# Kernel tuning notes

Hardware: AMD Instinct MI355X
Metric: run time of the kernel (lower is better)

## Reference

```python
import jax, jax.numpy as jnp
import numpy as np

E = 8          # num_experts
TOP_K = 2      # num_experts_per_tok
H = 1024       # hidden_size
F = 2048       # intermediate_size
B, S = 2, 4096


def setup_inputs() -> dict:
    key = jax.random.key(0)
    ks = jax.random.split(key, 5)
    hidden_states = jax.random.normal(ks[0], (B, S, H), dtype=jnp.float32)
    gate_w = jax.random.normal(ks[1], (E, H), dtype=jnp.float32) * 0.02   # router: logits = x @ gate_w.T
    Wg = jax.random.normal(ks[2], (E, H, F), dtype=jnp.float32) * 0.02    # gate_proj per expert
    Wu = jax.random.normal(ks[3], (E, H, F), dtype=jnp.float32) * 0.02    # up_proj per expert
    Wd = jax.random.normal(ks[4], (E, F, H), dtype=jnp.float32) * 0.02    # down_proj per expert
    return {"hidden_states": hidden_states, "gate_w": gate_w, "Wg": Wg, "Wu": Wu, "Wd": Wd}


def reference(hidden_states, gate_w, Wg, Wu, Wd):
    b, s, h = hidden_states.shape
    x = hidden_states.reshape(-1, h)                       # [T, H]
    T = x.shape[0]

    router_logits = x @ gate_w.T                           # [T, E]
    probs = jax.nn.softmax(router_logits.astype(jnp.float32), axis=-1)
    topk_w, topk_idx = jax.lax.top_k(probs, TOP_K)         # [T, K]
    topk_w = topk_w / jnp.sum(topk_w, axis=-1, keepdims=True)  # norm_topk_prob
    topk_w = topk_w.astype(x.dtype)

    # Dense per-token-per-expert combine weight (0 for unselected experts).
    w_full = jnp.zeros((T, E), dtype=x.dtype)
    w_full = w_full.at[jnp.arange(T)[:, None], topk_idx].add(topk_w)  # [T, E]

    out = jnp.zeros_like(x)
    for e in range(E):  # fixed small loop over experts
        g = jax.nn.silu(x @ Wg[e]) * (x @ Wu[e])           # [T, F]
        out = out + w_full[:, e:e + 1] * (g @ Wd[e])       # [T, H]

    return out.reshape(b, s, h), router_logits
```

## Files before the change

### kernel.cpp

```cpp
#include <hip/hip_runtime.h>
#include <cstdint>

#define NTOK   8192
#define HDIM   1024
#define FDIM   2048
#define NEXP   8
#define RTOT   (2*NTOK)
#define RPAD   128

typedef unsigned short u16;
typedef short   bf16x8 __attribute__((ext_vector_type(8)));
typedef float   f32x4  __attribute__((ext_vector_type(4)));
typedef u16     u16x8  __attribute__((ext_vector_type(8)));

__device__ __forceinline__ u16 f2bf(float v) {
  union { float f; uint32_t u; } a; a.f = v;
  uint32_t r = a.u + 0x7FFFu + ((a.u >> 16) & 1u);
  return (u16)(r >> 16);
}
__device__ __forceinline__ float bf2f(u16 b) {
  union { uint32_t u; float f; } a; a.u = ((uint32_t)b) << 16; return a.f;
}

__global__ void router_kernel(const float* __restrict__ x, const float* __restrict__ gw,
                              float* __restrict__ logits, int* __restrict__ te,
                              float* __restrict__ tw) {
  int gid  = blockIdx.x * blockDim.x + threadIdx.x;
  int t    = gid >> 6;
  int lane = gid & 63;
  const float4* xr = (const float4*)(x + (size_t)t * HDIM);
  float acc[NEXP];
#pragma unroll
  for (int e = 0; e < NEXP; ++e) acc[e] = 0.f;
#pragma unroll
  for (int c = 0; c < 4; ++c) {
    float4 xv = xr[c * 64 + lane];
#pragma unroll
    for (int e = 0; e < NEXP; ++e) {
      float4 wv = ((const float4*)(gw + e * HDIM))[c * 64 + lane];
      acc[e] += xv.x * wv.x + xv.y * wv.y + xv.z * wv.z + xv.w * wv.w;
    }
  }
#pragma unroll
  for (int off = 32; off > 0; off >>= 1)
#pragma unroll
    for (int e = 0; e < NEXP; ++e) acc[e] += __shfl_xor(acc[e], off, 64);

  if (lane == 0) {
#pragma unroll
    for (int e = 0; e < NEXP; ++e) logits[(size_t)t * NEXP + e] = acc[e];
    int e1 = 0;
#pragma unroll
    for (int e = 1; e < NEXP; ++e) if (acc[e] > acc[e1]) e1 = e;
    int e2 = -1;
#pragma unroll
    for (int e = 0; e < NEXP; ++e) {
      if (e == e1) continue;
      if (e2 < 0 || acc[e] > acc[e2]) e2 = e;
    }
    float m  = fmaxf(acc[e1], acc[e2]);
    float p1 = __expf(acc[e1] - m), p2 = __expf(acc[e2] - m);
    float inv = 1.f / (p1 + p2);
    te[t * 2]     = e1;  tw[t * 2]     = p1 * inv;
    te[t * 2 + 1] = e2;  tw[t * 2 + 1] = p2 * inv;
  }
}

__global__ void count_prefix_kernel(const int* __restrict__ te, int* __restrict__ offs,
                                    int* __restrict__ cursors) {
  __shared__ int wsum[16][NEXP];
  int cnt[NEXP];
#pragma unroll
  for (int e = 0; e < NEXP; ++e) cnt[e] = 0;
  for (int i = threadIdx.x; i < 2 * NTOK; i += 1024) {
    int v = te[i];
#pragma unroll
    for (int e = 0; e < NEXP; ++e) cnt[e] += (v == e) ? 1 : 0;
  }
#pragma unroll
  for (int off = 32; off > 0; off >>= 1)
#pragma unroll
    for (int e = 0; e < NEXP; ++e) cnt[e] += __shfl_xor(cnt[e], off, 64);
  int wave = threadIdx.x >> 6, lane = threadIdx.x & 63;
  if (lane == 0)
#pragma unroll
    for (int e = 0; e < NEXP; ++e) wsum[wave][e] = cnt[e];
  __syncthreads();
  if (threadIdx.x == 0) {
    int s = 0;
    for (int e = 0; e < NEXP; ++e) {
      int c = 0;
      for (int w = 0; w < 16; ++w) c += wsum[w][e];
      offs[e] = s; cursors[e * 16] = s; s += c;
    }
    offs[NEXP] = s;
  }
}

__global__ void scatter_kernel(const int* __restrict__ te, const float* __restrict__ tw,
                               int* __restrict__ cursors, int* __restrict__ tok_ids,
                               float* __restrict__ wts, int* __restrict__ slots) {
  int t    = blockIdx.x * blockDim.x + threadIdx.x;
  int lane = threadIdx.x & 63;
#pragma unroll
  for (int s = 0; s < 2; ++s) {
    int   e = te[t * 2 + s];
    float w = tw[t * 2 + s];
    int pos = 0;
#pragma unroll
    for (int e0 = 0; e0 < NEXP; ++e0) {
      unsigned long long m = __ballot(e == e0);
      if (e == e0) {
        int leader = __ffsll((unsigned long long)m) - 1;
        int rank   = __popcll(m & ((1ull << lane) - 1ull));
        int b = 0;
        if (lane == leader) b = atomicAdd(&cursors[e0 * 16], (int)__popcll(m));
        b = __shfl(b, leader, 64);
        pos = b + rank;
      }
    }
    tok_ids[pos] = t;
    wts[pos] = w;
    slots[t * 2 + s] = pos;
  }
}

__global__ void gather_cast_kernel(const float* __restrict__ x, const int* __restrict__ tok_ids,
                                   u16* __restrict__ Xg) {
  int j = blockIdx.x;
  int t = tok_ids[j];
  float4 v = ((const float4*)(x + (size_t)t * HDIM))[threadIdx.x];
  ushort4 o;
  o.x = f2bf(v.x); o.y = f2bf(v.y); o.z = f2bf(v.z); o.w = f2bf(v.w);
  ((ushort4*)(Xg + (size_t)j * HDIM))[threadIdx.x] = o;
}

__global__ __launch_bounds__(256)
void prep_weights_kernel(const float* __restrict__ Wg, const float* __restrict__ Wu,
                         const float* __restrict__ Wd, u16* __restrict__ Wgt,
                         u16* __restrict__ Wut, u16* __restrict__ Wdt) {
  __shared__ float tile[64 * 65];
  const int mat = blockIdx.z >> 3;
  const int e   = blockIdx.z & 7;
  const int K   = (mat < 2) ? HDIM : FDIM;
  const int N   = (mat < 2) ? FDIM : HDIM;
  const float* src = ((mat == 0) ? Wg : (mat == 1) ? Wu : Wd) + (size_t)e * K * N;
  u16*         dst = ((mat == 0) ? Wgt : (mat == 1) ? Wut : Wdt) + (size_t)e * K * N;
  const int tn = (mat < 2) ? blockIdx.x : blockIdx.y;
  const int tk = (mat < 2) ? blockIdx.y : blockIdx.x;
  const int k0 = tk * 64, n0 = tn * 64;

  const int r  = threadIdx.x >> 2;
  const int c4 = threadIdx.x & 3;
#pragma unroll
  for (int i = 0; i < 4; ++i) {
    int c = (c4 + i * 4) * 4;
    float4 v = *(const float4*)(src + (size_t)(k0 + r) * N + n0 + c);
    tile[r * 65 + c]     = v.x;
    tile[r * 65 + c + 1] = v.y;
    tile[r * 65 + c + 2] = v.z;
    tile[r * 65 + c + 3] = v.w;
  }
  __syncthreads();

  const int kq = threadIdx.x & 7;
  const int nr = threadIdx.x >> 3;
#pragma unroll
  for (int p = 0; p < 2; ++p) {
    int n = p * 32 + nr;
    u16x8 pk;
#pragma unroll
    for (int j = 0; j < 8; ++j)
      pk[j] = f2bf(tile[(kq * 8 + j) * 65 + n]);
    *(u16x8*)(dst + (size_t)(n0 + n) * K + k0 + kq * 8) = pk;
  }
}

__device__ __forceinline__ void stage_tile(const u16* __restrict__ src, int ld,
                                           u16* __restrict__ lds, int wave, int lane) {
#pragma unroll
  for (int i = 0; i < 4; ++i) {
    int chunk = ((i << 2) + wave) << 9;
    int flat  = chunk + (lane << 3);
    int row   = flat >> 6;
    int km    = (flat & 63) ^ ((row & 7) << 3);
    __builtin_amdgcn_global_load_lds(
        (const __attribute__((address_space(1))) uint32_t*)(src + (size_t)row * ld + km),
        (__attribute__((address_space(3))) uint32_t*)(lds + chunk),
        16, 0, 0);
  }
}

__global__ __launch_bounds__(256, 2)
void gemm1_kernel(const u16* __restrict__ Xg, const u16* __restrict__ Wgt,
                  const u16* __restrict__ Wut, const int* __restrict__ offs,
                  u16* __restrict__ G) {
  const int e     = blockIdx.z;
  const int rbase = offs[e];
  const int rows  = offs[e + 1] - rbase;
  const int row0  = blockIdx.y * 128;
  if (row0 >= rows) return;
  const int n0    = blockIdx.x * 128;
  const int arow0 = rbase + row0;

  __shared__ __align__(16) u16 As[128 * 64];
  __shared__ __align__(16) u16 Bgs[128 * 64];
  __shared__ __align__(16) u16 Bus[128 * 64];

  const int tid  = threadIdx.x;
  const int wave = tid >> 6;
  const int lane = tid & 63;
  const int wm   = wave >> 1, wn = wave & 1;
  const int l15  = lane & 15, quad = lane >> 4;

  const u16* Ag = Xg  + (size_t)arow0 * HDIM;
  const u16* Bg = Wgt + (size_t)e * FDIM * HDIM + (size_t)n0 * HDIM;
  const u16* Bu = Wut + (size_t)e * FDIM * HDIM + (size_t)n0 * HDIM;

  f32x4 accg[4][4], accu[4][4];
#pragma unroll
  for (int i = 0; i < 4; ++i)
#pragma unroll
    for (int j = 0; j < 4; ++j) { accg[i][j] = (f32x4)0.f; accu[i][j] = (f32x4)0.f; }

  for (int kt = 0; kt < HDIM / 64; ++kt) {
    const int k0 = kt * 64;
    stage_tile(Ag + k0, HDIM, As,  wave, lane);
    stage_tile(Bg + k0, HDIM, Bgs, wave, lane);
    stage_tile(Bu + k0, HDIM, Bus, wave, lane);
    __syncthreads();
#pragma unroll
    for (int kk = 0; kk < 64; kk += 32) {
      bf16x8 af[4];
#pragma unroll
      for (int im = 0; im < 4; ++im) {
        int r  = wm * 64 + im * 16 + l15;
        int kq = (kk + quad * 8) ^ ((r & 7) << 3);
        af[im] = *(const bf16x8*)(As + r * 64 + kq);
      }
#pragma unroll
      for (int in = 0; in < 4; ++in) {
        int r  = wn * 64 + in * 16 + l15;
        int kq = (kk + quad * 8) ^ ((r & 7) << 3);
        bf16x8 bg = *(const bf16x8*)(Bgs + r * 64 + kq);
        bf16x8 bu = *(const bf16x8*)(Bus + r * 64 + kq);
#pragma unroll
        for (int im = 0; im < 4; ++im) {
          accg[im][in] = __builtin_amdgcn_mfma_f32_16x16x32_bf16(af[im], bg, accg[im][in], 0, 0, 0);
          accu[im][in] = __builtin_amdgcn_mfma_f32_16x16x32_bf16(af[im], bu, accu[im][in], 0, 0, 0);
        }
      }
    }
    __syncthreads();
  }

#pragma unroll
  for (int im = 0; im < 4; ++im) {
#pragma unroll
    for (int rr = 0; rr < 4; ++rr) {
      int lrow = row0 + wm * 64 + im * 16 + quad * 4 + rr;
      if (lrow < rows) {
        size_t grow = (size_t)(rbase + lrow);
#pragma unroll
        for (int in = 0; in < 4; ++in) {
          float g = accg[im][in][rr];
          float u = accu[im][in][rr];
          float val = g / (1.f + __expf(-g)) * u;
          int gcol = n0 + wn * 64 + in * 16 + l15;
          G[grow * FDIM + gcol] = f2bf(val);
        }
      }
    }
  }
}

__global__ __launch_bounds__(256, 2)
void gemm2_kernel(const u16* __restrict__ G, const u16* __restrict__ Wdt,
                  const int* __restrict__ offs, const float* __restrict__ wts,
                  u16* __restrict__ Y) {
  const int e     = blockIdx.z;
  const int rbase = offs[e];
  const int rows  = offs[e + 1] - rbase;
  const int row0  = blockIdx.y * 128;
  if (row0 >= rows) return;
  const int n0    = blockIdx.x * 128;
  const int arow0 = rbase + row0;

  __shared__ __align__(16) u16 As[128 * 64];
  __shared__ __align__(16) u16 Bs[128 * 64];

  const int tid  = threadIdx.x;
  const int wave = tid >> 6;
  const int lane = tid & 63;
  const int wm   = wave >> 1, wn = wave & 1;
  const int l15  = lane & 15, quad = lane >> 4;

  const u16* Ag = G   + (size_t)arow0 * FDIM;
  const u16* Bg = Wdt + (size_t)e * HDIM * FDIM + (size_t)n0 * FDIM;

  f32x4 acc[4][4];
#pragma unroll
  for (int i = 0; i < 4; ++i)
#pragma unroll
    for (int j = 0; j < 4; ++j) acc[i][j] = (f32x4)0.f;

  for (int kt = 0; kt < FDIM / 64; ++kt) {
    const int k0 = kt * 64;
    stage_tile(Ag + k0, FDIM, As, wave, lane);
    stage_tile(Bg + k0, FDIM, Bs, wave, lane);
    __syncthreads();
#pragma unroll
    for (int kk = 0; kk < 64; kk += 32) {
      bf16x8 af[4], bf[4];
#pragma unroll
      for (int im = 0; im < 4; ++im) {
        int r  = wm * 64 + im * 16 + l15;
        int kq = (kk + quad * 8) ^ ((r & 7) << 3);
        af[im] = *(const bf16x8*)(As + r * 64 + kq);
      }
#pragma unroll
      for (int in = 0; in < 4; ++in) {
        int r  = wn * 64 + in * 16 + l15;
        int kq = (kk + quad * 8) ^ ((r & 7) << 3);
        bf[in] = *(const bf16x8*)(Bs + r * 64 + kq);
      }
#pragma unroll
      for (int in = 0; in < 4; ++in)
#pragma unroll
        for (int im = 0; im < 4; ++im)
          acc[im][in] = __builtin_amdgcn_mfma_f32_16x16x32_bf16(af[im], bf[in], acc[im][in], 0, 0, 0);
    }
    __syncthreads();
  }

#pragma unroll
  for (int im = 0; im < 4; ++im) {
#pragma unroll
    for (int rr = 0; rr < 4; ++rr) {
      int lrow = row0 + wm * 64 + im * 16 + quad * 4 + rr;
      if (lrow < rows) {
        int grow = rbase + lrow;
        float w  = wts[grow];
        u16* yrow = Y + (size_t)grow * HDIM + n0 + wn * 64 + l15;
#pragma unroll
        for (int in = 0; in < 4; ++in)
          yrow[in * 16] = f2bf(acc[im][in][rr] * w);
      }
    }
  }
}

__global__ void combine_kernel(const u16* __restrict__ Y, const int* __restrict__ slots,
                               float* __restrict__ out) {
  int t  = blockIdx.x;
  int s1 = slots[2 * t], s2 = slots[2 * t + 1];
  ushort4 a = ((const ushort4*)(Y + (size_t)s1 * HDIM))[threadIdx.x];
  ushort4 b = ((const ushort4*)(Y + (size_t)s2 * HDIM))[threadIdx.x];
  float4 o;
  o.x = bf2f(a.x) + bf2f(b.x);
  o.y = bf2f(a.y) + bf2f(b.y);
  o.z = bf2f(a.z) + bf2f(b.z);
  o.w = bf2f(a.w) + bf2f(b.w);
  ((float4*)(out + (size_t)t * HDIM))[threadIdx.x] = o;
}

extern "C" void kernel_launch(void* const* d_in, const int* in_sizes, int n_in,
                              void* d_out, int out_size, void* d_ws, size_t ws_size,
                              hipStream_t stream) {
  const float* x  = (const float*)d_in[0];
  const float* gw = (const float*)d_in[1];
  const float* Wg = (const float*)d_in[2];
  const float* Wu = (const float*)d_in[3];
  const float* Wd = (const float*)d_in[4];

  float* out    = (float*)d_out;
  float* logits = out + (size_t)NTOK * HDIM;

  char* p = (char*)d_ws;
  u16* Wgt = (u16*)p;  p += (size_t)NEXP * FDIM * HDIM * 2;
  u16* Wut = (u16*)p;  p += (size_t)NEXP * FDIM * HDIM * 2;
  u16* Wdt = (u16*)p;  p += (size_t)NEXP * HDIM * FDIM * 2;
  u16* Xg  = (u16*)p;  p += (size_t)(RTOT + RPAD) * HDIM * 2;
  u16* G   = (u16*)p;  p += (size_t)(RTOT + RPAD) * FDIM * 2;
  int*   tok_ids = (int*)p;   p += (RTOT + RPAD) * 4;
  float* wts     = (float*)p; p += (RTOT + RPAD) * 4;
  int*   te      = (int*)p;   p += NTOK * 2 * 4;
  float* tw      = (float*)p; p += NTOK * 2 * 4;
  int*   slots   = (int*)p;   p += NTOK * 2 * 4;
  int*   offs    = (int*)p;   p += (NEXP + 1) * 4;
  int*   cursors = (int*)p;   p += NEXP * 16 * 4;

  u16* Y = Xg;

  router_kernel<<<(NTOK * 64) / 256, 256, 0, stream>>>(x, gw, logits, te, tw);
  count_prefix_kernel<<<1, 1024, 0, stream>>>(te, offs, cursors);
  scatter_kernel<<<NTOK / 256, 256, 0, stream>>>(te, tw, cursors, tok_ids, wts, slots);
  gather_cast_kernel<<<RTOT, 256, 0, stream>>>(x, tok_ids, Xg);

  prep_weights_kernel<<<dim3(32, 16, 24), 256, 0, stream>>>(Wg, Wu, Wd, Wgt, Wut, Wdt);

  gemm1_kernel<<<dim3(FDIM / 128, 64, NEXP), 256, 0, stream>>>(Xg, Wgt, Wut, offs, G);
  gemm2_kernel<<<dim3(HDIM / 128, 64, NEXP), 256, 0, stream>>>(G, Wdt, offs, wts, Y);
  combine_kernel<<<NTOK, 256, 0, stream>>>(Y, slots, out);
}
```

Baseline: 556.3 us.

## Fuse bf16 cast into router and gather rows inside gemm1 via token indices

```diff
diff --git a/kernel.cpp b/kernel.cpp
--- a/kernel.cpp
+++ b/kernel.cpp
@@ -24,22 +24,29 @@
 
 __global__ void router_kernel(const float* __restrict__ x, const float* __restrict__ gw,
                               float* __restrict__ logits, int* __restrict__ te,
-                              float* __restrict__ tw) {
+                              float* __restrict__ tw, u16* __restrict__ Xb) {
   int gid  = blockIdx.x * blockDim.x + threadIdx.x;
   int t    = gid >> 6;
   int lane = gid & 63;
   const float4* xr = (const float4*)(x + (size_t)t * HDIM);
+  float4 xv[4];
   float acc[NEXP];
 #pragma unroll
   for (int e = 0; e < NEXP; ++e) acc[e] = 0.f;
 #pragma unroll
   for (int c = 0; c < 4; ++c) {
-    float4 xv = xr[c * 64 + lane];
+    xv[c] = xr[c * 64 + lane];
 #pragma unroll
     for (int e = 0; e < NEXP; ++e) {
       float4 wv = ((const float4*)(gw + e * HDIM))[c * 64 + lane];
-      acc[e] += xv.x * wv.x + xv.y * wv.y + xv.z * wv.z + xv.w * wv.w;
-    }
+      acc[e] += xv[c].x * wv.x + xv[c].y * wv.y + xv[c].z * wv.z + xv[c].w * wv.w;
+    }
+  }
+#pragma unroll
+  for (int c = 0; c < 4; ++c) {
+    ushort4 o;
+    o.x = f2bf(xv[c].x); o.y = f2bf(xv[c].y); o.z = f2bf(xv[c].z); o.w = f2bf(xv[c].w);
+    ((ushort4*)(Xb + (size_t)t * HDIM))[c * 64 + lane] = o;
   }
 #pragma unroll
   for (int off = 32; off > 0; off >>= 1)
@@ -123,16 +130,6 @@
     wts[pos] = w;
     slots[t * 2 + s] = pos;
   }
-}
-
-__global__ void gather_cast_kernel(const float* __restrict__ x, const int* __restrict__ tok_ids,
-                                   u16* __restrict__ Xg) {
-  int j = blockIdx.x;
-  int t = tok_ids[j];
-  float4 v = ((const float4*)(x + (size_t)t * HDIM))[threadIdx.x];
-  ushort4 o;
-  o.x = f2bf(v.x); o.y = f2bf(v.y); o.z = f2bf(v.z); o.w = f2bf(v.w);
-  ((ushort4*)(Xg + (size_t)j * HDIM))[threadIdx.x] = o;
 }
 
 __global__ __launch_bounds__(256)
@@ -191,10 +188,10 @@
   }
 }
 
-__global__ __launch_bounds__(256, 2)
-void gemm1_kernel(const u16* __restrict__ Xg, const u16* __restrict__ Wgt,
-                  const u16* __restrict__ Wut, const int* __restrict__ offs,
-                  u16* __restrict__ G) {
+__global__ __launch_bounds__(256, 3)
+void gemm1_kernel(const u16* __restrict__ Xb, const int* __restrict__ tok_ids,
+                  const u16* __restrict__ Wgt, const u16* __restrict__ Wut,
+                  const int* __restrict__ offs, u16* __restrict__ G) {
   const int e     = blockIdx.z;
   const int rbase = offs[e];
   const int rows  = offs[e + 1] - rbase;
@@ -213,7 +210,17 @@
   const int wm   = wave >> 1, wn = wave & 1;
   const int l15  = lane & 15, quad = lane >> 4;
 
-  const u16* Ag = Xg  + (size_t)arow0 * HDIM;
+  const u16* aoff[4];
+#pragma unroll
+  for (int i = 0; i < 4; ++i) {
+    int chunk = ((i << 2) + wave) << 9;
+    int flat  = chunk + (lane << 3);
+    int row   = flat >> 6;
+    int km    = (flat & 63) ^ ((row & 7) << 3);
+    int idx   = arow0 + row; idx = (idx < RTOT) ? idx : (RTOT - 1);
+    aoff[i] = Xb + (size_t)tok_ids[idx] * HDIM + km;
+  }
+
   const u16* Bg = Wgt + (size_t)e * FDIM * HDIM + (size_t)n0 * HDIM;
   const u16* Bu = Wut + (size_t)e * FDIM * HDIM + (size_t)n0 * HDIM;
 
@@ -225,7 +232,13 @@
 
   for (int kt = 0; kt < HDIM / 64; ++kt) {
     const int k0 = kt * 64;
-    stage_tile(Ag + k0, HDIM, As,  wave, lane);
+#pragma unroll
+    for (int i = 0; i < 4; ++i) {
+      int chunk = ((i << 2) + wave) << 9;
+      __builtin_amdgcn_global_load_lds(
+          (const __attribute__((address_space(1))) uint32_t*)(aoff[i] + k0),
+          (__attribute__((address_space(3))) uint32_t*)(As + chunk), 16, 0, 0);
+    }
     stage_tile(Bg + k0, HDIM, Bgs, wave, lane);
     stage_tile(Bu + k0, HDIM, Bus, wave, lane);
     __syncthreads();
@@ -274,7 +287,7 @@
   }
 }
 
-__global__ __launch_bounds__(256, 2)
+__global__ __launch_bounds__(256, 4)
 void gemm2_kernel(const u16* __restrict__ G, const u16* __restrict__ Wdt,
                   const int* __restrict__ offs, const float* __restrict__ wts,
                   u16* __restrict__ Y) {
@@ -380,8 +393,9 @@
   u16* Wgt = (u16*)p;  p += (size_t)NEXP * FDIM * HDIM * 2;
   u16* Wut = (u16*)p;  p += (size_t)NEXP * FDIM * HDIM * 2;
   u16* Wdt = (u16*)p;  p += (size_t)NEXP * HDIM * FDIM * 2;
-  u16* Xg  = (u16*)p;  p += (size_t)(RTOT + RPAD) * HDIM * 2;
+  u16* Xb  = (u16*)p;  p += (size_t)NTOK * HDIM * 2;
   u16* G   = (u16*)p;  p += (size_t)(RTOT + RPAD) * FDIM * 2;
+  u16* Y   = (u16*)p;  p += (size_t)(RTOT + RPAD) * HDIM * 2;
   int*   tok_ids = (int*)p;   p += (RTOT + RPAD) * 4;
   float* wts     = (float*)p; p += (RTOT + RPAD) * 4;
   int*   te      = (int*)p;   p += NTOK * 2 * 4;
@@ -390,16 +404,13 @@
   int*   offs    = (int*)p;   p += (NEXP + 1) * 4;
   int*   cursors = (int*)p;   p += NEXP * 16 * 4;
 
-  u16* Y = Xg;
-
-  router_kernel<<<(NTOK * 64) / 256, 256, 0, stream>>>(x, gw, logits, te, tw);
+  router_kernel<<<(NTOK * 64) / 256, 256, 0, stream>>>(x, gw, logits, te, tw, Xb);
   count_prefix_kernel<<<1, 1024, 0, stream>>>(te, offs, cursors);
   scatter_kernel<<<NTOK / 256, 256, 0, stream>>>(te, tw, cursors, tok_ids, wts, slots);
-  gather_cast_kernel<<<RTOT, 256, 0, stream>>>(x, tok_ids, Xg);
 
   prep_weights_kernel<<<dim3(32, 16, 24), 256, 0, stream>>>(Wg, Wu, Wd, Wgt, Wut, Wdt);
 
-  gemm1_kernel<<<dim3(FDIM / 128, 64, NEXP), 256, 0, stream>>>(Xg, Wgt, Wut, offs, G);
+  gemm1_kernel<<<dim3(FDIM / 128, 64, NEXP), 256, 0, stream>>>(Xb, tok_ids, Wgt, Wut, offs, G);
   gemm2_kernel<<<dim3(HDIM / 128, 64, NEXP), 256, 0, stream>>>(G, Wdt, offs, wts, Y);
   combine_kernel<<<NTOK, 256, 0, stream>>>(Y, slots, out);
 }
```

New measurement: 626.3 us. 1.13x slower.
